# Kernel optimization log

Measured on AMD Instinct MI355X. Metric: run time of the kernel, lower is better.

Reference implementation:

```python
import jax, jax.numpy as jnp
import numpy as np

N, M, D = 2048, 100000, 128
K = 5


def setup_inputs() -> dict:
    key = jax.random.key(0)
    k1, k2 = jax.random.split(key)
    features = jax.random.normal(k1, (N, D), dtype=jnp.float32)
    memory_bank = jax.random.normal(k2, (M, D), dtype=jnp.float32)
    # normalization buffers computed during fit(); use plausible scalars
    min_val = jnp.zeros((), dtype=jnp.float32)
    max_val = jnp.ones((), dtype=jnp.float32)
    return {
        "features": features,
        "memory_bank": memory_bank,
        "min_val": min_val,
        "max_val": max_val,
        "n_neighbors": K,
    }


def reference(features, memory_bank, min_val, max_val, n_neighbors):
    x2 = jnp.sum(features * features, axis=1, keepdims=True)        # (N,1)
    y2 = jnp.sum(memory_bank * memory_bank, axis=1)[None, :]        # (1,M)
    d2 = x2 + y2 - 2.0 * (features @ memory_bank.T)                 # (N,M)
    dist = jnp.sqrt(jnp.maximum(d2, 0.0))
    # k smallest distances per query (topk largest=False)
    neg_knn, _ = jax.lax.top_k(-dist, n_neighbors)                  # (N,K)
    knn = -neg_knn
    # min-max normalization with fitted stats
    knn = (knn - min_val) / (max_val - min_val)
    return knn.mean(axis=1)                                         # (N,)
```

## Files before the change

### kernel.cpp

```cpp
#include <hip/hip_runtime.h>
#include <stdint.h>

#define N_Q 2048
#define M_B 100000
#define D_DIM 128
#define KNN 5
#define SLABS_TOTAL 1563
#define M_PAD (SLABS_TOTAL * 64)
#define CHUNKS 96
#define SPC 17
#define CLS 16
#define FTOT (CHUNKS * CLS)
#define ROWBLOCKS 8
#define TROWS 256
#define BIGF 3.0e38f
#define NEGF -3.0e38f


typedef __attribute__((ext_vector_type(8))) short short8;
typedef __attribute__((ext_vector_type(4))) unsigned short ushort4v;
typedef __attribute__((ext_vector_type(8))) unsigned short ushort8v;
typedef __attribute__((ext_vector_type(4))) float f32x4;

static __device__ __forceinline__ unsigned short f2bf(float f) {
  unsigned int u = __builtin_bit_cast(unsigned int, f);
  u = (u + 0x7FFFu + ((u >> 16) & 1u)) >> 16;
  return (unsigned short)u;
}

static __device__ __forceinline__ void gload_lds16(const void* g, void* l) {
  __builtin_amdgcn_global_load_lds((const __attribute__((address_space(1))) unsigned int*)g,
                                   (__attribute__((address_space(3))) unsigned int*)l, 16, 0, 0);
}
static __device__ __forceinline__ void gload_lds4(const void* g, void* l) {
  __builtin_amdgcn_global_load_lds((const __attribute__((address_space(1))) unsigned int*)g,
                                   (__attribute__((address_space(3))) unsigned int*)l, 4, 0, 0);
}

#define DPPADD(v, ctrl)                                                              \
  do {                                                                               \
    int _t = __builtin_amdgcn_update_dpp(0, __builtin_bit_cast(int, (v)), (ctrl),    \
                                         0xf, 0xf, false);                           \
    (v) = (v) + __builtin_bit_cast(float, _t);                                       \
  } while (0)

__global__ __launch_bounds__(256) void k_prep(const float* __restrict__ Y,
                                              unsigned short* __restrict__ ybf,
                                              float* __restrict__ ny2) {
  const int s = blockIdx.x;
  const int t = threadIdx.x;
  __shared__ __align__(16) unsigned short tile[8192];
  __shared__ float redy[64 * 33];
#pragma unroll
  for (int i = 0; i < 8; ++i) {
    const int u = i * 256 + t;
    const int rowl = u >> 5;
    const int q = u & 31;
    const int rowg = s * 64 + rowl;
    const int rowc = (rowg < M_B) ? rowg : (M_B - 1);
    const float4 v = ((const float4*)Y)[(size_t)rowc * 32 + q];
    redy[rowl * 33 + q] = v.x * v.x + v.y * v.y + v.z * v.z + v.w * v.w;
    ushort4v o;
    o[0] = f2bf(v.x); o[1] = f2bf(v.y); o[2] = f2bf(v.z); o[3] = f2bf(v.w);
    *(ushort4v*)(tile + (size_t)(((q >> 1) * 64 + rowl) * 8 + (q & 1) * 4)) = o;
  }
  __syncthreads();
  {
    const int rowl = t >> 2;
    const int k = t & 3;
    float ss = 0.f;
#pragma unroll
    for (int j = 0; j < 8; ++j) ss += redy[rowl * 33 + k * 8 + j];
    DPPADD(ss, 0xB1);
    DPPADD(ss, 0x4E);
    const int rowg = s * 64 + rowl;
    if ((t & 3) == 0) ny2[(size_t)s * 64 + rowl] = (rowg < M_B) ? (-0.5f * ss) : NEGF;
  }
#pragma unroll
  for (int i = 0; i < 4; ++i) {
    const int u = i * 256 + t;
    *(ushort8v*)(ybf + ((size_t)s * 1024 + u) * 8) = *(const ushort8v*)(tile + u * 8);
  }
}

__global__ __launch_bounds__(256, 3) void k_main(const float* __restrict__ X,
                                                 const unsigned short* __restrict__ ybf,
                                                 const float* __restrict__ ny2,
                                                 float* __restrict__ rsm) {
  __shared__ __align__(16) char smem[37120];
  unsigned short* ys = (unsigned short*)smem;
  float* ny2s = (float*)(smem + 32768);

  const int bid = blockIdx.x;
  const int chunk = bid % CHUNKS;
  const int rowblock = bid / CHUNKS;
  const int row0 = rowblock * TROWS;

  const int cs0 = chunk * SPC;
  int nslab = SLABS_TOTAL - cs0;
  if (nslab > SPC) nslab = SPC;
  if (nslab < 0) nslab = 0;

  const int t = threadIdx.x;
  const int wave = t >> 6;
  const int lane = t & 63;
  const int lm = lane & 15;
  const int lq = lane >> 4;

  short8 afrag[4][4];
#pragma unroll
  for (int rt = 0; rt < 4; ++rt)
#pragma unroll
    for (int ks = 0; ks < 4; ++ks) {
      const float* xr = X + (size_t)(row0 + wave * 64 + rt * 16 + lm) * D_DIM + ks * 32 + lq * 8;
      const float4 a = *(const float4*)xr;
      const float4 b = *(const float4*)(xr + 4);
      short8 f;
      f[0] = (short)f2bf(a.x); f[1] = (short)f2bf(a.y);
      f[2] = (short)f2bf(a.z); f[3] = (short)f2bf(a.w);
      f[4] = (short)f2bf(b.x); f[5] = (short)f2bf(b.y);
      f[6] = (short)f2bf(b.z); f[7] = (short)f2bf(b.w);
      afrag[rt][ks] = f;
    }

  for (int j = wave; j < nslab; j += 4)
    gload_lds4(ny2 + (size_t)(cs0 + j) * 64 + lane, ny2s + (size_t)j * 64);
  __syncthreads();

  float prmax[4][4];
#pragma unroll
  for (int rt = 0; rt < 4; ++rt)
#pragma unroll
    for (int rr = 0; rr < 4; ++rr) prmax[rt][rr] = NEGF;

  if (nslab > 0) {
    const unsigned short* src = ybf + (size_t)cs0 * 8192;
#pragma unroll
    for (int i = 0; i < 4; ++i) {
      const int ub = i * 256 + wave * 64;
      gload_lds16(src + (size_t)(ub + lane) * 8, ys + (size_t)ub * 8);
    }
  }

  for (int s = 0; s < nslab; ++s) {
    const unsigned short* yb = ys + (size_t)((s & 1) * 8192);
    if (s + 1 < nslab) {
      const unsigned short* src = ybf + (size_t)(cs0 + s + 1) * 8192;
      unsigned short* dst = ys + (size_t)(((s + 1) & 1) * 8192);
#pragma unroll
      for (int i = 0; i < 4; ++i) {
        const int ub = i * 256 + wave * 64;
        gload_lds16(src + (size_t)(ub + lane) * 8, dst + (size_t)ub * 8);
      }
      asm volatile("s_waitcnt vmcnt(4)" ::: "memory");
    } else {
      asm volatile("s_waitcnt vmcnt(0)" ::: "memory");
    }
    __builtin_amdgcn_s_barrier();

#pragma unroll
    for (int ct = 0; ct < 4; ++ct) {
      const float yc = ny2s[s * 64 + ct * 16 + lm];

      short8 bfr[4];
#pragma unroll
      for (int ks = 0; ks < 4; ++ks)
        bfr[ks] = *(const short8*)(yb + (size_t)(((ks * 4 + lq) * 64 + ct * 16 + lm)) * 8);

      f32x4 acc[4];
#pragma unroll
      for (int rt = 0; rt < 4; ++rt)
#pragma unroll
        for (int rr = 0; rr < 4; ++rr) acc[rt][rr] = yc;

#pragma unroll
      for (int ks = 0; ks < 4; ++ks)
#pragma unroll
        for (int rt = 0; rt < 4; ++rt)
          acc[rt] = __builtin_amdgcn_mfma_f32_16x16x32_bf16(afrag[rt][ks], bfr[ks],
                                                            acc[rt], 0, 0, 0);

#pragma unroll
      for (int rt = 0; rt < 4; ++rt)
#pragma unroll
        for (int rr = 0; rr < 4; ++rr)
          prmax[rt][rr] = fmaxf(prmax[rt][rr], acc[rt][rr]);
    }

    __builtin_amdgcn_s_barrier();
  }

#pragma unroll
  for (int rt = 0; rt < 4; ++rt)
#pragma unroll
    for (int rr = 0; rr < 4; ++rr) {
      const int lrow = wave * 64 + rt * 16 + lq * 4 + rr;
      rsm[(size_t)(row0 + lrow) * FTOT + chunk * CLS + lm] = prmax[rt][rr];
    }
}

__global__ __launch_bounds__(256) void k_scan(const float* __restrict__ rsm,
                                              const float* __restrict__ X,
                                              const float* __restrict__ minp,
                                              const float* __restrict__ maxp,
                                              float* __restrict__ out) {
  const int wave = threadIdx.x >> 6;
  const int lane = threadIdx.x & 63;
  const int row = blockIdx.x * 4 + wave;
  const float* rp = rsm + (size_t)row * FTOT;

  float x2;
  {
    const float a = X[(size_t)row * D_DIM + lane];
    const float b = X[(size_t)row * D_DIM + 64 + lane];
    x2 = a * a + b * b;
#pragma unroll
    for (int off = 1; off < 64; off <<= 1) x2 += __shfl_xor(x2, off);
  }

  float t0 = NEGF, t1 = NEGF, t2 = NEGF, t3 = NEGF, t4 = NEGF;
  for (int i = lane; i < FTOT; i += 64) {
    const float v = rp[i];
    if (v > t4) {
      float m = v;
      float n3 = fminf(t3, m); m = fmaxf(t3, m);
      float n2 = fminf(t2, m); m = fmaxf(t2, m);
      float n1 = fminf(t1, m); m = fmaxf(t1, m);
      float n0 = fminf(t0, m); m = fmaxf(t0, m);
      t0 = m; t1 = n0; t2 = n1; t3 = n2; t4 = n3;
    }
  }

  int k = 0;
  float sum = 0.f;
#pragma unroll
  for (int r = 0; r < KNN; ++r) {
    float head = (k == 0) ? t0 : (k == 1) ? t1 : (k == 2) ? t2 : (k == 3) ? t3
               : (k == 4) ? t4 : NEGF;
    float m = head;
#pragma unroll
    for (int off = 1; off < 64; off <<= 1) m = fmaxf(m, __shfl_xor(m, off));
    const unsigned long long mask = __ballot(head == m);
    const int first = __ffsll(mask) - 1;
    if (lane == first) ++k;
    sum += sqrtf(fmaxf(x2 - 2.f * m, 0.f));
  }
  if (lane == 0) {
    const float mn = minp[0], mx = maxp[0];
    out[row] = (sum * (1.0f / KNN) - mn) / (mx - mn);
  }
}

extern "C" void kernel_launch(void* const* d_in, const int* in_sizes, int n_in,
                              void* d_out, int out_size, void* d_ws, size_t ws_size,
                              hipStream_t stream) {
  const float* X = (const float*)d_in[0];
  const float* Y = (const float*)d_in[1];
  const float* minp = (const float*)d_in[2];
  const float* maxp = (const float*)d_in[3];
  float* out = (float*)d_out;

  char* ws = (char*)d_ws;
  size_t off = 0;
  unsigned short* ybf = (unsigned short*)(ws + off); off += (size_t)M_PAD * D_DIM * 2;
  float* ny2 = (float*)(ws + off);                   off += (size_t)M_PAD * 4;
  float* rsm = (float*)(ws + off);                   off += (size_t)N_Q * FTOT * 4;

  k_prep<<<dim3(SLABS_TOTAL), dim3(256), 0, stream>>>(Y, ybf, ny2);
  k_main<<<dim3(ROWBLOCKS * CHUNKS), dim3(256), 0, stream>>>(X, ybf, ny2, rsm);
  k_scan<<<dim3(N_Q / 4), dim3(256), 0, stream>>>(rsm, X, minp, maxp, out);
}
```

Measured before the change: 150.1 us.

## Fuse memory-bank bf16 conversion and norm computation into main kernel

Removes the separate prep kernel that converted the memory bank to bf16 and computed its squared norms. The main kernel now loads fp32 rows directly, converts them to bf16 into LDS, and computes partial norms per slab, prefetching the next slab with register loads between compute steps. This saves a kernel launch and the workspace write and re-read. In exchange, each of the 8 row blocks repeats the conversion, fp32 global traffic doubles, and the asynchronous global-to-LDS pipeline becomes synchronous register loads that may expose latency.

```diff
diff --git a/kernel.cpp b/kernel.cpp
--- a/kernel.cpp
+++ b/kernel.cpp
@@ -6,19 +6,16 @@
 #define D_DIM 128
 #define KNN 5
 #define SLABS_TOTAL 1563
-#define M_PAD (SLABS_TOTAL * 64)
 #define CHUNKS 96
 #define SPC 17
 #define CLS 16
 #define FTOT (CHUNKS * CLS)
 #define ROWBLOCKS 8
 #define TROWS 256
-#define BIGF 3.0e38f
 #define NEGF -3.0e38f
 
 
 typedef __attribute__((ext_vector_type(8))) short short8;
-typedef __attribute__((ext_vector_type(4))) unsigned short ushort4v;
 typedef __attribute__((ext_vector_type(8))) unsigned short ushort8v;
 typedef __attribute__((ext_vector_type(4))) float f32x4;
 
@@ -28,68 +25,12 @@
   return (unsigned short)u;
 }
 
-static __device__ __forceinline__ void gload_lds16(const void* g, void* l) {
-  __builtin_amdgcn_global_load_lds((const __attribute__((address_space(1))) unsigned int*)g,
-                                   (__attribute__((address_space(3))) unsigned int*)l, 16, 0, 0);
-}
-static __device__ __forceinline__ void gload_lds4(const void* g, void* l) {
-  __builtin_amdgcn_global_load_lds((const __attribute__((address_space(1))) unsigned int*)g,
-                                   (__attribute__((address_space(3))) unsigned int*)l, 4, 0, 0);
-}
-
-#define DPPADD(v, ctrl)                                                              \
-  do {                                                                               \
-    int _t = __builtin_amdgcn_update_dpp(0, __builtin_bit_cast(int, (v)), (ctrl),    \
-                                         0xf, 0xf, false);                           \
-    (v) = (v) + __builtin_bit_cast(float, _t);                                       \
-  } while (0)
-
-__global__ __launch_bounds__(256) void k_prep(const float* __restrict__ Y,
-                                              unsigned short* __restrict__ ybf,
-                                              float* __restrict__ ny2) {
-  const int s = blockIdx.x;
-  const int t = threadIdx.x;
-  __shared__ __align__(16) unsigned short tile[8192];
-  __shared__ float redy[64 * 33];
-#pragma unroll
-  for (int i = 0; i < 8; ++i) {
-    const int u = i * 256 + t;
-    const int rowl = u >> 5;
-    const int q = u & 31;
-    const int rowg = s * 64 + rowl;
-    const int rowc = (rowg < M_B) ? rowg : (M_B - 1);
-    const float4 v = ((const float4*)Y)[(size_t)rowc * 32 + q];
-    redy[rowl * 33 + q] = v.x * v.x + v.y * v.y + v.z * v.z + v.w * v.w;
-    ushort4v o;
-    o[0] = f2bf(v.x); o[1] = f2bf(v.y); o[2] = f2bf(v.z); o[3] = f2bf(v.w);
-    *(ushort4v*)(tile + (size_t)(((q >> 1) * 64 + rowl) * 8 + (q & 1) * 4)) = o;
-  }
-  __syncthreads();
-  {
-    const int rowl = t >> 2;
-    const int k = t & 3;
-    float ss = 0.f;
-#pragma unroll
-    for (int j = 0; j < 8; ++j) ss += redy[rowl * 33 + k * 8 + j];
-    DPPADD(ss, 0xB1);
-    DPPADD(ss, 0x4E);
-    const int rowg = s * 64 + rowl;
-    if ((t & 3) == 0) ny2[(size_t)s * 64 + rowl] = (rowg < M_B) ? (-0.5f * ss) : NEGF;
-  }
-#pragma unroll
-  for (int i = 0; i < 4; ++i) {
-    const int u = i * 256 + t;
-    *(ushort8v*)(ybf + ((size_t)s * 1024 + u) * 8) = *(const ushort8v*)(tile + u * 8);
-  }
-}
-
 __global__ __launch_bounds__(256, 3) void k_main(const float* __restrict__ X,
-                                                 const unsigned short* __restrict__ ybf,
-                                                 const float* __restrict__ ny2,
+                                                 const float* __restrict__ Y,
                                                  float* __restrict__ rsm) {
-  __shared__ __align__(16) char smem[37120];
+  __shared__ __align__(16) char smem[34816];
   unsigned short* ys = (unsigned short*)smem;
-  float* ny2s = (float*)(smem + 32768);
+  float* pny = (float*)(smem + 32768);
 
   const int bid = blockIdx.x;
   const int chunk = bid % CHUNKS;
@@ -123,49 +64,50 @@
       afrag[rt][ks] = f;
     }
 
-  for (int j = wave; j < nslab; j += 4)
-    gload_lds4(ny2 + (size_t)(cs0 + j) * 64 + lane, ny2s + (size_t)j * 64);
+  float prmax[4][4];
+#pragma unroll
+  for (int rt = 0; rt < 4; ++rt)
+#pragma unroll
+    for (int rr = 0; rr < 4; ++rr) prmax[rt][rr] = NEGF;
+
+  if (nslab > 0) {
+    const int g = cs0 * 64 + lane;
+    const int gc = (g < M_B) ? g : (M_B - 1);
+    const float* yrp = Y + (size_t)gc * D_DIM;
+    float part = 0.f;
+#pragma unroll
+    for (int i = 0; i < 4; ++i) {
+      const int kc = i * 4 + wave;
+      const float4 a = *(const float4*)(yrp + kc * 8);
+      const float4 b = *(const float4*)(yrp + kc * 8 + 4);
+      part += a.x * a.x + a.y * a.y + a.z * a.z + a.w * a.w
+            + b.x * b.x + b.y * b.y + b.z * b.z + b.w * b.w;
+      ushort8v o;
+      o[0] = f2bf(a.x); o[1] = f2bf(a.y); o[2] = f2bf(a.z); o[3] = f2bf(a.w);
+      o[4] = f2bf(b.x); o[5] = f2bf(b.y); o[6] = f2bf(b.z); o[7] = f2bf(b.w);
+      *(ushort8v*)(ys + (size_t)(kc * 64 + lane) * 8) = o;
+    }
+    pny[wave * 64 + lane] = part;
+  }
   __syncthreads();
 
-  float prmax[4][4];
-#pragma unroll
-  for (int rt = 0; rt < 4; ++rt)
-#pragma unroll
-    for (int rr = 0; rr < 4; ++rr) prmax[rt][rr] = NEGF;
-
-  if (nslab > 0) {
-    const unsigned short* src = ybf + (size_t)cs0 * 8192;
-#pragma unroll
-    for (int i = 0; i < 4; ++i) {
-      const int ub = i * 256 + wave * 64;
-      gload_lds16(src + (size_t)(ub + lane) * 8, ys + (size_t)ub * 8);
-    }
-  }
-
+  int cur = 0;
   for (int s = 0; s < nslab; ++s) {
-    const unsigned short* yb = ys + (size_t)((s & 1) * 8192);
-    if (s + 1 < nslab) {
-      const unsigned short* src = ybf + (size_t)(cs0 + s + 1) * 8192;
-      unsigned short* dst = ys + (size_t)(((s + 1) & 1) * 8192);
-#pragma unroll
-      for (int i = 0; i < 4; ++i) {
-        const int ub = i * 256 + wave * 64;
-        gload_lds16(src + (size_t)(ub + lane) * 8, dst + (size_t)ub * 8);
-      }
-      asm volatile("s_waitcnt vmcnt(4)" ::: "memory");
-    } else {
-      asm volatile("s_waitcnt vmcnt(0)" ::: "memory");
-    }
-    __builtin_amdgcn_s_barrier();
+    const unsigned short* yb = ys + (size_t)cur * 8192;
+    const float* pb = pny + cur * 256;
+    const int sg = cs0 + s;
 
 #pragma unroll
     for (int ct = 0; ct < 4; ++ct) {
-      const float yc = ny2s[s * 64 + ct * 16 + lm];
+      const int r = ct * 16 + lm;
+      const float sum = pb[r] + pb[64 + r] + pb[128 + r] + pb[192 + r];
+      const int yrow = sg * 64 + r;
+      const float yc = (yrow < M_B) ? (-0.5f * sum) : NEGF;
 
       short8 bfr[4];
 #pragma unroll
       for (int ks = 0; ks < 4; ++ks)
-        bfr[ks] = *(const short8*)(yb + (size_t)(((ks * 4 + lq) * 64 + ct * 16 + lm)) * 8);
+        bfr[ks] = *(const short8*)(yb + (size_t)(((ks * 4 + lq) * 64 + r)) * 8);
 
       f32x4 acc[4];
 #pragma unroll
@@ -187,7 +129,29 @@
           prmax[rt][rr] = fmaxf(prmax[rt][rr], acc[rt][rr]);
     }
 
-    __builtin_amdgcn_s_barrier();
+    if (s + 1 < nslab) {
+      const int g = (sg + 1) * 64 + lane;
+      const int gc = (g < M_B) ? g : (M_B - 1);
+      const float* yrp = Y + (size_t)gc * D_DIM;
+      unsigned short* dst = ys + (size_t)(cur ^ 1) * 8192;
+      float part = 0.f;
+#pragma unroll
+      for (int i = 0; i < 4; ++i) {
+        const int kc = i * 4 + wave;
+        const float4 a = *(const float4*)(yrp + kc * 8);
+        const float4 b = *(const float4*)(yrp + kc * 8 + 4);
+        part += a.x * a.x + a.y * a.y + a.z * a.z + a.w * a.w
+              + b.x * b.x + b.y * b.y + b.z * b.z + b.w * b.w;
+        ushort8v o;
+        o[0] = f2bf(a.x); o[1] = f2bf(a.y); o[2] = f2bf(a.z); o[3] = f2bf(a.w);
+        o[4] = f2bf(b.x); o[5] = f2bf(b.y); o[6] = f2bf(b.z); o[7] = f2bf(b.w);
+        *(ushort8v*)(dst + (size_t)(kc * 64 + lane) * 8) = o;
+      }
+      pny[(cur ^ 1) * 256 + wave * 64 + lane] = part;
+    }
+
+    __syncthreads();
+    cur ^= 1;
   }
 
 #pragma unroll
@@ -260,13 +224,8 @@
   const float* maxp = (const float*)d_in[3];
   float* out = (float*)d_out;
 
-  char* ws = (char*)d_ws;
-  size_t off = 0;
-  unsigned short* ybf = (unsigned short*)(ws + off); off += (size_t)M_PAD * D_DIM * 2;
-  float* ny2 = (float*)(ws + off);                   off += (size_t)M_PAD * 4;
-  float* rsm = (float*)(ws + off);                   off += (size_t)N_Q * FTOT * 4;
-
-  k_prep<<<dim3(SLABS_TOTAL), dim3(256), 0, stream>>>(Y, ybf, ny2);
-  k_main<<<dim3(ROWBLOCKS * CHUNKS), dim3(256), 0, stream>>>(X, ybf, ny2, rsm);
+  float* rsm = (float*)d_ws;
+
+  k_main<<<dim3(ROWBLOCKS * CHUNKS), dim3(256), 0, stream>>>(X, Y, rsm);
   k_scan<<<dim3(N_Q / 4), dim3(256), 0, stream>>>(rsm, X, minp, maxp, out);
 }
```

Result: slower. 211.3 us (+40.7%).
